# Optimization experiments

Hardware: AMD Instinct MI355X
Metric: run time of the kernel (lower is better)

## Reference

```python
import jax, jax.numpy as jnp
import numpy as np

B, T, C = 8, 2048, 1024


def setup_inputs() -> dict:
    key = jax.random.key(0)
    ks = jax.random.split(key, 7)
    s = 0.02  # typical init scale for weights
    return {
        "x": jax.random.normal(ks[0], (B, T, C), jnp.float32),
        "wq": jax.random.normal(ks[1], (C, C), jnp.float32) * s,
        "bq": jax.random.normal(ks[2], (C,), jnp.float32) * s,
        "wk": jax.random.normal(ks[3], (C, C), jnp.float32) * s,
        "bk": jax.random.normal(ks[4], (C,), jnp.float32) * s,
        "wv": jax.random.normal(ks[5], (C, C), jnp.float32) * s,
        "bv": jax.random.normal(ks[6], (C,), jnp.float32) * s,
    }


def reference(x, wq, bq, wk, bk, wv, bv):
    # x: [B, T, C]; torch Linear stores weight as [out, in] -> x @ W.T + b
    Bx, Tx, Cx = x.shape
    Q = x @ wq.T + bq  # [B, T, C]
    K = x @ wk.T + bk
    V = x @ wv.T + bv
    # NOTE: source computes K @ Q^T (keys index rows, queries index columns)
    scores = jnp.einsum("btc,bsc->bts", K, Q) / jnp.sqrt(jnp.float32(Cx))  # [B, T, T]
    causal = jnp.tril(jnp.ones((Tx, Tx), dtype=bool))  # mask==0 above diagonal
    scores = jnp.where(causal, scores, -jnp.inf)
    # torch masked_fill with a (1,1,T,T) mask broadcasts scores to (1,B,T,T)
    scores = scores[None]  # [1, B, T, T]
    w = jax.nn.softmax(scores, axis=-1)
    out = jnp.einsum("abts,bsc->abtc", w, V)  # [1, B, T, C]
    return out
```

## Files before the change

### kernel.cpp

```cpp
#include <hip/hip_runtime.h>
#include <stdint.h>

typedef unsigned short u16;
typedef __attribute__((ext_vector_type(8))) __bf16 bf16x8;
typedef __attribute__((ext_vector_type(4))) float f32x4;

#define DEVI __device__ __forceinline__

DEVI u16 f32_to_bf16(float f) {
  uint32_t u = __builtin_bit_cast(uint32_t, f);
  u += 0x7FFFu + ((u >> 16) & 1u);
  return (u16)(u >> 16);
}

DEVI void gl2lds16(const void* g, void* l) {
  __builtin_amdgcn_global_load_lds(
      (const __attribute__((address_space(1))) void*)g,
      (__attribute__((address_space(3))) void*)l, 16, 0, 0);
}

#define SMEM_U16 17408

#define S_BATCH 2228224

DEVI void gemm_bt_mainloop(const u16* __restrict__ A, const u16* __restrict__ B,
                           int lda, int ldb, int kIters,
                           u16* As, u16* Bs, f32x4 (&acc)[4][4]) {
  const int tid = threadIdx.x;
  const int lane = tid & 63;
  const int wid = tid >> 6;
  const int wr = wid >> 1, wc = wid & 1;
  const int l15 = lane & 15, quad = lane >> 4;

  const int srow = tid >> 3;
  const int sgrp = ((tid & 7) - srow) & 7;
  const u16* Ag = A + (size_t)srow * lda + sgrp * 8;
  const u16* Bg = B + (size_t)srow * ldb + sgrp * 8;
  char* AsDst = (char*)As + tid * 16;
  char* BsDst = (char*)Bs + tid * 16;

  const int a_row0 = wr * 64 + l15;
  const int b_row0 = wc * 64 + l15;

  for (int kb = 0; kb < kIters; ++kb) {
#pragma unroll
    for (int r = 0; r < 4; ++r) {
      gl2lds16(Ag + (size_t)(r * 32) * lda, AsDst + r * 4096);
      gl2lds16(Bg + (size_t)(r * 32) * ldb, BsDst + r * 4096);
    }
    Ag += 64;
    Bg += 64;
    __syncthreads();
#pragma unroll
    for (int kk = 0; kk < 2; ++kk) {
      const int gA = ((kk * 4 + quad + a_row0) & 7) * 8;
      const int gB = ((kk * 4 + quad + b_row0) & 7) * 8;
      bf16x8 af[4], bfr[4];
#pragma unroll
      for (int i = 0; i < 4; ++i)
        af[i] = *(const bf16x8*)(As + (a_row0 + i * 16) * 64 + gA);
#pragma unroll
      for (int j = 0; j < 4; ++j)
        bfr[j] = *(const bf16x8*)(Bs + (b_row0 + j * 16) * 64 + gB);
#pragma unroll
      for (int i = 0; i < 4; ++i)
#pragma unroll
        for (int j = 0; j < 4; ++j)
          acc[i][j] = __builtin_amdgcn_mfma_f32_16x16x32_bf16(af[i], bfr[j],
                                                              acc[i][j], 0, 0, 0);
    }
    __syncthreads();
  }
}

__global__ void cast_f32_to_bf16_kernel(const float* __restrict__ src,
                                        u16* __restrict__ dst, int n4) {
  int i = blockIdx.x * blockDim.x + threadIdx.x;
  const int stride = gridDim.x * blockDim.x;
  for (; i < n4; i += stride) {
    const float4 v = ((const float4*)src)[i];
    ushort4 o;
    o.x = f32_to_bf16(v.x);
    o.y = f32_to_bf16(v.y);
    o.z = f32_to_bf16(v.z);
    o.w = f32_to_bf16(v.w);
    ((ushort4*)dst)[i] = o;
  }
}

__global__ void cast_w_kernel(const float* __restrict__ wq,
                              const float* __restrict__ wk,
                              const float* __restrict__ wv,
                              u16* __restrict__ wb, float* __restrict__ sums) {
  const int z = blockIdx.y;
  if (z == 3) {
    int i = blockIdx.x * blockDim.x + threadIdx.x;
    if (i < 4096) ((float4*)sums)[i] = (float4){0.f, 0.f, 0.f, 0.f};
    return;
  }
  const float* src = (z == 0) ? wq : (z == 1) ? wk : wv;
  u16* dst = wb + (size_t)z * 1048576;
  int i = blockIdx.x * blockDim.x + threadIdx.x;
  const int stride = gridDim.x * blockDim.x;
  for (; i < 262144; i += stride) {
    const float4 v = ((const float4*)src)[i];
    ushort4 o;
    o.x = f32_to_bf16(v.x);
    o.y = f32_to_bf16(v.y);
    o.z = f32_to_bf16(v.z);
    o.w = f32_to_bf16(v.w);
    ((ushort4*)dst)[i] = o;
  }
}

__global__ __launch_bounds__(512, 2) void qkv_kernel(
    const u16* __restrict__ xb, const u16* __restrict__ wb,
    const float* __restrict__ bq, const float* __restrict__ bk,
    const float* __restrict__ bv, u16* __restrict__ Qb, u16* __restrict__ Kb,
    u16* __restrict__ Vt) {
  __shared__ __align__(16) u16 lds[65536];

  const int id = blockIdx.x;
  const int wg = (id & 7) * 96 + (id >> 3);
  const int g = wg >> 3, u = wg & 7;
  const int z = g >> 5;
  const int tp = g & 31;
  const int tmt = tp * 2 + (u >> 2);
  const int tct = u & 3;

  int m0, n0;
  const u16* Aptr;
  const u16* Bptr;
  if (z < 2) {
    m0 = tct * 256;
    n0 = tmt * 256;
    Aptr = wb + (size_t)z * 1048576 + (size_t)m0 * 1024;
    Bptr = xb + (size_t)n0 * 1024;
  } else {
    m0 = tmt * 256;
    n0 = tct * 256;
    Aptr = xb + (size_t)m0 * 1024;
    Bptr = wb + (size_t)2 * 1048576 + (size_t)n0 * 1024;
  }

  const int tid = threadIdx.x;
  const int srow = tid >> 3;
  const int sgrp = ((tid & 7) - srow) & 7;
  const u16* Ag = Aptr + (size_t)srow * 1024 + sgrp * 8;
  const u16* Bg = Bptr + (size_t)srow * 1024 + sgrp * 8;
  char* ldsDst = (char*)lds + tid * 16;

#define ST_A0(kt) do { const u16* s_ = Ag + (kt) * 64;           char* d_ = ldsDst + (((kt) & 1) * 65536);         gl2lds16(s_, d_); gl2lds16(s_ + 65536, d_ + 8192); } while (0)
#define ST_A1(kt) do { const u16* s_ = Ag + 131072 + (kt) * 64;  char* d_ = ldsDst + (((kt) & 1) * 65536) + 16384; gl2lds16(s_, d_); gl2lds16(s_ + 65536, d_ + 8192); } while (0)
#define ST_B0(kt) do { const u16* s_ = Bg + (kt) * 64;           char* d_ = ldsDst + (((kt) & 1) * 65536) + 32768; gl2lds16(s_, d_); gl2lds16(s_ + 65536, d_ + 8192); } while (0)
#define ST_B1(kt) do { const u16* s_ = Bg + 131072 + (kt) * 64;  char* d_ = ldsDst + (((kt) & 1) * 65536) + 49152; gl2lds16(s_, d_); gl2lds16(s_ + 65536, d_ + 8192); } while (0)

  ST_A0(0); ST_B0(0); ST_B1(0); ST_A1(0);
  ST_A0(1); ST_B0(1); ST_B1(1);

  const int lane = tid & 63, wid = tid >> 6;
  const int wr = wid >> 2, wc = wid & 3;
  const int l15 = lane & 15, quad = lane >> 4;

  int aoff[4][2], boff[2][2];
#pragma unroll
  for (int i_ = 0; i_ < 4; ++i_) {
    const int arow = wr * 64 + i_ * 16 + l15;
#pragma unroll
    for (int k_ = 0; k_ < 2; ++k_)
      aoff[i_][k_] = arow * 64 + ((k_ * 4 + quad + arow) & 7) * 8;
  }
#pragma unroll
  for (int j_ = 0; j_ < 2; ++j_) {
    const int brow = wc * 32 + j_ * 16 + l15;
#pragma unroll
    for (int k_ = 0; k_ < 2; ++k_)
      boff[j_][k_] = brow * 64 + ((k_ * 4 + quad + brow) & 7) * 8;
  }

  f32x4 acc[2][2][4][2];
#pragma unroll
  for (int a_ = 0; a_ < 2; ++a_)
#pragma unroll
    for (int b_ = 0; b_ < 2; ++b_)
#pragma unroll
      for (int i_ = 0; i_ < 4; ++i_)
#pragma unroll
        for (int j_ = 0; j_ < 2; ++j_)
          acc[a_][b_][i_][j_] = (f32x4){0.f, 0.f, 0.f, 0.f};

  bf16x8 af[4][2], bfr[2][2][2];

#define LOADA(qm, buf) do { const u16* p_ = lds + (buf) * 32768 + (qm) * 8192; \
  _Pragma("unroll") for (int i_ = 0; i_ < 4; ++i_) \
  _Pragma("unroll") for (int k_ = 0; k_ < 2; ++k_) \
    af[i_][k_] = *(const bf16x8*)(p_ + aoff[i_][k_]); } while (0)
#define LOADB(qn, buf) do { const u16* p_ = lds + (buf) * 32768 + 16384 + (qn) * 8192; \
  _Pragma("unroll") for (int j_ = 0; j_ < 2; ++j_) \
  _Pragma("unroll") for (int k_ = 0; k_ < 2; ++k_) \
    bfr[qn][j_][k_] = *(const bf16x8*)(p_ + boff[j_][k_]); } while (0)
#define MMA(qm, qn) do { \
  _Pragma("unroll") for (int i_ = 0; i_ < 4; ++i_) \
  _Pragma("unroll") for (int j_ = 0; j_ < 2; ++j_) \
  _Pragma("unroll") for (int k_ = 0; k_ < 2; ++k_) \
    acc[qm][qn][i_][j_] = __builtin_amdgcn_mfma_f32_16x16x32_bf16( \
        af[i_][k_], bfr[qn][j_][k_], acc[qm][qn][i_][j_], 0, 0, 0); } while (0)

#define BAR __builtin_amdgcn_s_barrier()
#define WLG0 asm volatile("s_waitcnt lgkmcnt(0)")
#define PRIO1 __builtin_amdgcn_s_setprio(1)
#define PRIO0 __builtin_amdgcn_s_setprio(0)
#define WVM6 asm volatile("s_waitcnt vmcnt(6)" ::: "memory")
#define WVM0 asm volatile("s_waitcnt vmcnt(0)" ::: "memory")

  WVM6;
  BAR;

#pragma unroll 1
  for (int it = 0; it < 7; ++it) {
    const int j0 = 2 * it;
    LOADA(0, 0); LOADB(0, 0); ST_A1(j0 + 1);
    BAR; WLG0; PRIO1; MMA(0, 0); PRIO0; LOADB(1, 0); BAR;
    ST_A0(j0 + 2);
    BAR; WLG0; PRIO1; MMA(0, 1); PRIO0; LOADA(1, 0); BAR;
    ST_B0(j0 + 2);
    BAR; WLG0; PRIO1; MMA(1, 1); PRIO0; BAR;
    ST_B1(j0 + 2);
    BAR; PRIO1; MMA(1, 0); PRIO0;
    WVM6;
    BAR;
    LOADA(0, 1); LOADB(0, 1); ST_A1(j0 + 2);
    BAR; WLG0; PRIO1; MMA(0, 0); PRIO0; LOADB(1, 1); BAR;
    ST_A0(j0 + 3);
    BAR; WLG0; PRIO1; MMA(0, 1); PRIO0; LOADA(1, 1); BAR;
    ST_B0(j0 + 3);
    BAR; WLG0; PRIO1; MMA(1, 1); PRIO0; BAR;
    ST_B1(j0 + 3);
    BAR; PRIO1; MMA(1, 0); PRIO0;
    WVM6;
    BAR;
  }
  {
    LOADA(0, 0); LOADB(0, 0); ST_A1(15);
    BAR; WLG0; PRIO1; MMA(0, 0); PRIO0; LOADB(1, 0); BAR;
    BAR; WLG0; PRIO1; MMA(0, 1); PRIO0; LOADA(1, 0); BAR;
    BAR; WLG0; PRIO1; MMA(1, 1); PRIO0; BAR;
    BAR; PRIO1; MMA(1, 0); PRIO0;
    WVM0;
    BAR;
    LOADA(0, 1); LOADB(0, 1);
    BAR; WLG0; PRIO1; MMA(0, 0); PRIO0; LOADB(1, 1); BAR;
    BAR; WLG0; PRIO1; MMA(0, 1); PRIO0; LOADA(1, 1); BAR;
    BAR; WLG0; PRIO1; MMA(1, 1); PRIO0; BAR;
    PRIO1; MMA(1, 0); PRIO0;
  }

  if (z < 2) {
    const float* bias = (z == 0) ? bq : bk;
    u16* Out = (z == 0) ? Qb : Kb;
#pragma unroll
    for (int th = 0; th < 2; ++th) {
      if (th) __syncthreads();
#pragma unroll
      for (int qm = 0; qm < 2; ++qm)
#pragma unroll
        for (int i_ = 0; i_ < 4; ++i_) {
          const int c = qm * 128 + wr * 64 + i_ * 16 + quad * 4;
          const float4 b4 = *(const float4*)(bias + m0 + c);
#pragma unroll
          for (int j_ = 0; j_ < 2; ++j_) {
            const int row = wc * 32 + j_ * 16 + l15;
            ushort4 o;
            o.x = f32_to_bf16(acc[qm][th][i_][j_][0] + b4.x);
            o.y = f32_to_bf16(acc[qm][th][i_][j_][1] + b4.y);
            o.z = f32_to_bf16(acc[qm][th][i_][j_][2] + b4.z);
            o.w = f32_to_bf16(acc[qm][th][i_][j_][3] + b4.w);
            *(ushort4*)(lds + row * 264 + c) = o;
          }
        }
      __syncthreads();
#pragma unroll
      for (int p = 0; p < 8; ++p) {
        const int row = p * 16 + (tid >> 5);
        const int c0 = (tid & 31) * 8;
        const uint4 v = *(const uint4*)(lds + row * 264 + c0);
        *(uint4*)(Out + (size_t)(n0 + th * 128 + row) * 1024 + m0 + c0) = v;
      }
    }
  } else {
    const int b = m0 >> 11;
    const int t0b = m0 & 2047;
    u16* Out = Vt + (size_t)b * 2097152;
#pragma unroll
    for (int th = 0; th < 2; ++th) {
      if (th) __syncthreads();
#pragma unroll
      for (int j_ = 0; j_ < 2; ++j_) {
        const int row = wc * 32 + j_ * 16 + l15;
        const float bb = bv[n0 + th * 128 + row];
#pragma unroll
        for (int qm = 0; qm < 2; ++qm)
#pragma unroll
          for (int i_ = 0; i_ < 4; ++i_) {
            const int c = qm * 128 + wr * 64 + i_ * 16 + quad * 4;
            ushort4 o;
            o.x = f32_to_bf16(acc[qm][th][i_][j_][0] + bb);
            o.y = f32_to_bf16(acc[qm][th][i_][j_][1] + bb);
            o.z = f32_to_bf16(acc[qm][th][i_][j_][2] + bb);
            o.w = f32_to_bf16(acc[qm][th][i_][j_][3] + bb);
            *(ushort4*)(lds + row * 264 + c) = o;
          }
      }
      __syncthreads();
#pragma unroll
      for (int p = 0; p < 8; ++p) {
        const int row = p * 16 + (tid >> 5);
        const int c0 = (tid & 31) * 8;
        const uint4 v = *(const uint4*)(lds + row * 264 + c0);
        *(uint4*)(Out + (size_t)(n0 + th * 128 + row) * 2048 + t0b + c0) = v;
      }
    }
  }
#undef ST_A0
#undef ST_A1
#undef ST_B0
#undef ST_B1
#undef LOADA
#undef LOADB
#undef MMA
#undef BAR
#undef WLG0
#undef PRIO1
#undef PRIO0
#undef WVM6
#undef WVM0
}

__global__ __launch_bounds__(512, 2) void score_kernel(const u16* __restrict__ Kb,
                                                       const u16* __restrict__ Qb,
                                                       u16* __restrict__ Spk,
                                                       float* __restrict__ sums) {
  __shared__ __align__(16) u16 lds[49152];

  const int id = blockIdx.x;
  const int b = id & 7;
  const int l = id >> 3;
  int k = (int)((sqrtf(4.f * l + 1.f) - 1.f) * 0.5f);
  if (k * (k + 1) > l) --k;
  if ((k + 1) * (k + 2) <= l) ++k;
  const int off = l - k * (k + 1);
  const int hi = (off >= (k + 1));
  const int rt = 2 * k + hi;
  const int ct = off - (hi ? (k + 1) : 0);
  const bool maskT = (ct == k);

  const int tid = threadIdx.x;
  const int srow = tid >> 3;
  const int sgrp = ((tid & 7) - srow) & 7;
  const u16* A = Qb + ((size_t)b * 2048 + ct * 256) * 1024;
  const u16* B = Kb + ((size_t)b * 2048 + rt * 128) * 1024;
  const u16* Ag = A + (size_t)srow * 1024 + sgrp * 8;
  const u16* Bg = B + (size_t)srow * 1024 + sgrp * 8;
  char* ldsDst = (char*)lds + tid * 16;

#define ST_A0(kt) do { const u16* s_ = Ag + (kt) * 64;           char* d_ = ldsDst + (((kt) & 1) * 49152);         gl2lds16(s_, d_); gl2lds16(s_ + 65536, d_ + 8192); } while (0)
#define ST_A1(kt) do { const u16* s_ = Ag + 131072 + (kt) * 64;  char* d_ = ldsDst + (((kt) & 1) * 49152) + 16384; gl2lds16(s_, d_); gl2lds16(s_ + 65536, d_ + 8192); } while (0)
#define ST_B(kt)  do { const u16* s_ = Bg + (kt) * 64;           char* d_ = ldsDst + (((kt) & 1) * 49152) + 32768; gl2lds16(s_, d_); gl2lds16(s_ + 65536, d_ + 8192); } while (0)

  ST_A0(0); ST_B(0); ST_A1(0);
  ST_A0(1); ST_B(1);

  const int lane = tid & 63, wid = tid >> 6;
  const int wr = wid >> 2, wc = wid & 3;
  const int l15 = lane & 15, quad = lane >> 4;

  int aoff[4][2], boff[2][2];
#pragma unroll
  for (int i_ = 0; i_ < 4; ++i_) {
    const int arow = wr * 64 + i_ * 16 + l15;
#pragma unroll
    for (int k_ = 0; k_ < 2; ++k_)
      aoff[i_][k_] = arow * 64 + ((k_ * 4 + quad + arow) & 7) * 8;
  }
#pragma unroll
  for (int j_ = 0; j_ < 2; ++j_) {
    const int brow = wc * 32 + j_ * 16 + l15;
#pragma unroll
    for (int k_ = 0; k_ < 2; ++k_)
      boff[j_][k_] = brow * 64 + ((k_ * 4 + quad + brow) & 7) * 8;
  }

  f32x4 acc[2][4][2];
#pragma unroll
  for (int q_ = 0; q_ < 2; ++q_)
#pragma unroll
    for (int i_ = 0; i_ < 4; ++i_)
#pragma unroll
      for (int j_ = 0; j_ < 2; ++j_)
        acc[q_][i_][j_] = (f32x4){0.f, 0.f, 0.f, 0.f};

  bf16x8 af[4][2], bfr[2][2];

#define SLOADA(qm, buf) do { const u16* p_ = lds + (buf) * 24576 + (qm) * 8192; \
  _Pragma("unroll") for (int i_ = 0; i_ < 4; ++i_) \
  _Pragma("unroll") for (int k_ = 0; k_ < 2; ++k_) \
    af[i_][k_] = *(const bf16x8*)(p_ + aoff[i_][k_]); } while (0)
#define SLOADB(buf) do { const u16* p_ = lds + (buf) * 24576 + 16384; \
  _Pragma("unroll") for (int j_ = 0; j_ < 2; ++j_) \
  _Pragma("unroll") for (int k_ = 0; k_ < 2; ++k_) \
    bfr[j_][k_] = *(const bf16x8*)(p_ + boff[j_][k_]); } while (0)
#define SMMA(qm) do { \
  _Pragma("unroll") for (int i_ = 0; i_ < 4; ++i_) \
  _Pragma("unroll") for (int j_ = 0; j_ < 2; ++j_) \
  _Pragma("unroll") for (int k_ = 0; k_ < 2; ++k_) \
    acc[qm][i_][j_] = __builtin_amdgcn_mfma_f32_16x16x32_bf16( \
        af[i_][k_], bfr[j_][k_], acc[qm][i_][j_], 0, 0, 0); } while (0)

#define BAR __builtin_amdgcn_s_barrier()
#define WLG0 asm volatile("s_waitcnt lgkmcnt(0)")
#define PRIO1 __builtin_amdgcn_s_setprio(1)
#define PRIO0 __builtin_amdgcn_s_setprio(0)
#define WVM4 asm volatile("s_waitcnt vmcnt(4)" ::: "memory")
#define WVM0 asm volatile("s_waitcnt vmcnt(0)" ::: "memory")

  WVM4;
  BAR;

#pragma unroll 1
  for (int it = 0; it < 7; ++it) {
    const int j0 = 2 * it;
    SLOADA(0, 0); SLOADB(0); ST_A1(j0 + 1);
    BAR; WLG0; PRIO1; SMMA(0); PRIO0; SLOADA(1, 0); BAR;
    ST_A0(j0 + 2); ST_B(j0 + 2);
    BAR; WLG0; PRIO1; SMMA(1); PRIO0;
    WVM4;
    BAR;
    SLOADA(0, 1); SLOADB(1); ST_A1(j0 + 2);
    BAR; WLG0; PRIO1; SMMA(0); PRIO0; SLOADA(1, 1); BAR;
    ST_A0(j0 + 3); ST_B(j0 + 3);
    BAR; WLG0; PRIO1; SMMA(1); PRIO0;
    WVM4;
    BAR;
  }
  {
    SLOADA(0, 0); SLOADB(0); ST_A1(15);
    BAR; WLG0; PRIO1; SMMA(0); PRIO0; SLOADA(1, 0); BAR;
    BAR; WLG0; PRIO1; SMMA(1); PRIO0;
    WVM0;
    BAR;
    SLOADA(0, 1); SLOADB(1);
    BAR; WLG0; PRIO1; SMMA(0); PRIO0; SLOADA(1, 1); BAR;
    BAR; WLG0; PRIO1; SMMA(1); PRIO0; BAR;
  }

  const int moff = (rt & 1) * 128;
  float sj[2] = {0.f, 0.f};
#pragma unroll
  for (int qm = 0; qm < 2; ++qm)
#pragma unroll
    for (int i_ = 0; i_ < 4; ++i_) {
      const int s0 = qm * 128 + wr * 64 + i_ * 16 + quad * 4;
#pragma unroll
      for (int j_ = 0; j_ < 2; ++j_) {
        const int t = wc * 32 + j_ * 16 + l15;
        ushort4 o;
        float e[4];
#pragma unroll
        for (int r = 0; r < 4; ++r) {
          float v = __expf(acc[qm][i_][j_][r] * 0.03125f);
          if (maskT && (s0 + r) > (t + moff)) v = 0.f;
          e[r] = v;
          sj[j_] += v;
        }
        o.x = f32_to_bf16(e[0]);
        o.y = f32_to_bf16(e[1]);
        o.z = f32_to_bf16(e[2]);
        o.w = f32_to_bf16(e[3]);
        *(ushort4*)(lds + t * 264 + s0) = o;
      }
    }
#pragma unroll
  for (int j_ = 0; j_ < 2; ++j_) {
    float v = sj[j_];
    v += __shfl_xor(v, 16);
    v += __shfl_xor(v, 32);
    if (quad == 0)
      atomicAdd(&sums[(size_t)b * 2048 + rt * 128 + wc * 32 + j_ * 16 + l15], v);
  }
  __syncthreads();
  const int ld = (rt + 1) * 128;
  const int nc = ld - ct * 256;
  u16* Out = Spk + (size_t)b * S_BATCH + (size_t)(rt * (rt + 1) / 2) * 16384 +
             ct * 256;
  if (nc >= 256) {
#pragma unroll
    for (int p = 0; p < 8; ++p) {
      const int row = p * 16 + (tid >> 5);
      const int c0 = (tid & 31) * 8;
      const uint4 v = *(const uint4*)(lds + row * 264 + c0);
      *(uint4*)(Out + (size_t)row * ld + c0) = v;
    }
  } else {
#pragma unroll
    for (int p = 0; p < 4; ++p) {
      const int row = p * 32 + (tid >> 4);
      const int c0 = (tid & 15) * 8;
      const uint4 v = *(const uint4*)(lds + row * 264 + c0);
      *(uint4*)(Out + (size_t)row * ld + c0) = v;
    }
  }
#undef ST_A0
#undef ST_A1
#undef ST_B
#undef SLOADA
#undef SLOADB
#undef SMMA
#undef BAR
#undef WLG0
#undef PRIO1
#undef PRIO0
#undef WVM4
#undef WVM0
}

__global__ __launch_bounds__(256) void pv_kernel(const u16* __restrict__ Spk,
                                                 const u16* __restrict__ Vt,
                                                 const float* __restrict__ sums,
                                                 float* __restrict__ Out) {
  const int b = blockIdx.x & 7;
  const int local = 127 - (blockIdx.x >> 3);
  const int rt = local >> 3;
  const int ct = local & 7;

  __shared__ __align__(16) u16 smem[SMEM_U16];
  u16* As = smem;
  u16* Bs = smem + 8192;
  float* ftile = (float*)smem;

  f32x4 acc[4][4];
#pragma unroll
  for (int i = 0; i < 4; ++i)
#pragma unroll
    for (int j = 0; j < 4; ++j) acc[i][j] = (f32x4){0.f, 0.f, 0.f, 0.f};

  const u16* A = Vt + ((size_t)b * 1024 + ct * 128) * 2048;
  const u16* B = Spk + (size_t)b * S_BATCH +
                 (size_t)(rt * (rt + 1) / 2) * 16384;
  const int ldb = (rt + 1) * 128;
  gemm_bt_mainloop(A, B, 2048, ldb, (rt + 1) * 2, As, Bs, acc);

  const int tid = threadIdx.x;
  const int lane = tid & 63, wid = tid >> 6;
  const int wr = wid >> 1, wc = wid & 1;
  const int l15 = lane & 15, quad = lane >> 4;

  const float* sumsb = sums + (size_t)b * 2048 + rt * 128;
  float* Ob = Out + (size_t)b * 2048 * 1024 + (size_t)(rt * 128) * 1024 +
              ct * 128;
#pragma unroll
  for (int h = 0; h < 2; ++h) {
    if (wc == h) {
#pragma unroll
      for (int j = 0; j < 4; ++j) {
        const int tl = j * 16 + l15;
        const float iv = 1.0f / sumsb[h * 64 + tl];
#pragma unroll
        for (int i = 0; i < 4; ++i) {
          const int c0 = wr * 64 + i * 16 + quad * 4;
          float4 v;
          v.x = acc[i][j][0] * iv;
          v.y = acc[i][j][1] * iv;
          v.z = acc[i][j][2] * iv;
          v.w = acc[i][j][3] * iv;
          *(float4*)(ftile + tl * 132 + c0) = v;
        }
      }
    }
    __syncthreads();
#pragma unroll
    for (int rr = 0; rr < 8; ++rr) {
      const int row = rr * 8 + (tid >> 5);
      const int c0 = (tid & 31) * 4;
      const float4 v = *(const float4*)(ftile + row * 132 + c0);
      *(float4*)(Ob + (size_t)(h * 64 + row) * 1024 + c0) = v;
    }
    __syncthreads();
  }
}

extern "C" void kernel_launch(void* const* d_in, const int* in_sizes, int n_in,
                              void* d_out, int out_size, void* d_ws,
                              size_t ws_size, hipStream_t stream) {
  const float* x = (const float*)d_in[0];
  const float* wq = (const float*)d_in[1];
  const float* bq = (const float*)d_in[2];
  const float* wk = (const float*)d_in[3];
  const float* bk = (const float*)d_in[4];
  const float* wv = (const float*)d_in[5];
  const float* bv = (const float*)d_in[6];
  float* out = (float*)d_out;
  char* ws = (char*)d_ws;

  u16* Qb = (u16*)(ws);
  u16* Kb = (u16*)(ws + ((size_t)32 << 20));
  u16* Vt = (u16*)(ws + ((size_t)64 << 20));
  u16* Spk = (u16*)(ws + ((size_t)96 << 20));
  u16* xb = (u16*)(ws + ((size_t)96 << 20));
  float* sums = (float*)(ws + ((size_t)132 << 20));
  u16* wb = (u16*)(ws + ((size_t)134 << 20));

  cast_f32_to_bf16_kernel<<<16384, 256, 0, stream>>>(x, xb, 16777216 / 4);
  cast_w_kernel<<<dim3(512, 4), 256, 0, stream>>>(wq, wk, wv, wb, sums);

  qkv_kernel<<<768, 512, 0, stream>>>(xb, wb, bq, bk, bv, Qb, Kb, Vt);

  score_kernel<<<576, 512, 0, stream>>>(Kb, Qb, Spk, sums);

  pv_kernel<<<8 * 128, 256, 0, stream>>>(Spk, Vt, sums, out);
}
```

Baseline: 333.3 us.

## Rewrite PV kernel as pipelined 256x128 tile GEMM and reschedule LDS reads

The PV kernel is rewritten. The old version used 256-thread blocks with 128x128 tiles and a single-buffered mainloop. The new one uses 512-thread blocks with 256x128 tiles, double-buffered direct global-to-LDS loads, the vmcnt/barrier/priority pipelined schedule already used by the score kernel, and a paired heavy/light rt ordering across the grid. In the QKV and score kernels, LDS fragment reads for the next MMA now issue after the barrier instead of inside the priority-1 MMA section, with a partial lgkmcnt wait added. The intent is to overlap memory with MFMA and raise reuse in PV, at the cost of fewer, larger blocks and more register pressure.

```diff
diff --git a/kernel.cpp b/kernel.cpp
--- a/kernel.cpp
+++ b/kernel.cpp
@@ -19,59 +19,7 @@
       (__attribute__((address_space(3))) void*)l, 16, 0, 0);
 }
 
-#define SMEM_U16 17408
-
 #define S_BATCH 2228224
-
-DEVI void gemm_bt_mainloop(const u16* __restrict__ A, const u16* __restrict__ B,
-                           int lda, int ldb, int kIters,
-                           u16* As, u16* Bs, f32x4 (&acc)[4][4]) {
-  const int tid = threadIdx.x;
-  const int lane = tid & 63;
-  const int wid = tid >> 6;
-  const int wr = wid >> 1, wc = wid & 1;
-  const int l15 = lane & 15, quad = lane >> 4;
-
-  const int srow = tid >> 3;
-  const int sgrp = ((tid & 7) - srow) & 7;
-  const u16* Ag = A + (size_t)srow * lda + sgrp * 8;
-  const u16* Bg = B + (size_t)srow * ldb + sgrp * 8;
-  char* AsDst = (char*)As + tid * 16;
-  char* BsDst = (char*)Bs + tid * 16;
-
-  const int a_row0 = wr * 64 + l15;
-  const int b_row0 = wc * 64 + l15;
-
-  for (int kb = 0; kb < kIters; ++kb) {
-#pragma unroll
-    for (int r = 0; r < 4; ++r) {
-      gl2lds16(Ag + (size_t)(r * 32) * lda, AsDst + r * 4096);
-      gl2lds16(Bg + (size_t)(r * 32) * ldb, BsDst + r * 4096);
-    }
-    Ag += 64;
-    Bg += 64;
-    __syncthreads();
-#pragma unroll
-    for (int kk = 0; kk < 2; ++kk) {
-      const int gA = ((kk * 4 + quad + a_row0) & 7) * 8;
-      const int gB = ((kk * 4 + quad + b_row0) & 7) * 8;
-      bf16x8 af[4], bfr[4];
-#pragma unroll
-      for (int i = 0; i < 4; ++i)
-        af[i] = *(const bf16x8*)(As + (a_row0 + i * 16) * 64 + gA);
-#pragma unroll
-      for (int j = 0; j < 4; ++j)
-        bfr[j] = *(const bf16x8*)(Bs + (b_row0 + j * 16) * 64 + gB);
-#pragma unroll
-      for (int i = 0; i < 4; ++i)
-#pragma unroll
-        for (int j = 0; j < 4; ++j)
-          acc[i][j] = __builtin_amdgcn_mfma_f32_16x16x32_bf16(af[i], bfr[j],
-                                                              acc[i][j], 0, 0, 0);
-    }
-    __syncthreads();
-  }
-}
 
 __global__ void cast_f32_to_bf16_kernel(const float* __restrict__ src,
                                         u16* __restrict__ dst, int n4) {
@@ -208,6 +156,7 @@
 
 #define BAR __builtin_amdgcn_s_barrier()
 #define WLG0 asm volatile("s_waitcnt lgkmcnt(0)")
+#define WLG8 asm volatile("s_waitcnt lgkmcnt(8)")
 #define PRIO1 __builtin_amdgcn_s_setprio(1)
 #define PRIO0 __builtin_amdgcn_s_setprio(0)
 #define WVM6 asm volatile("s_waitcnt vmcnt(6)" ::: "memory")
@@ -219,21 +168,21 @@
 #pragma unroll 1
   for (int it = 0; it < 7; ++it) {
     const int j0 = 2 * it;
-    LOADA(0, 0); LOADB(0, 0); ST_A1(j0 + 1);
-    BAR; WLG0; PRIO1; MMA(0, 0); PRIO0; LOADB(1, 0); BAR;
-    ST_A0(j0 + 2);
-    BAR; WLG0; PRIO1; MMA(0, 1); PRIO0; LOADA(1, 0); BAR;
-    ST_B0(j0 + 2);
+    LOADA(0, 0); LOADB(0, 0); ST_A1(j0 + 1); WLG8;
+    BAR; WLG0; PRIO1; MMA(0, 0); PRIO0; BAR;
+    LOADB(1, 0); ST_A0(j0 + 2);
+    BAR; WLG0; PRIO1; MMA(0, 1); PRIO0; BAR;
+    LOADA(1, 0); ST_B0(j0 + 2);
     BAR; WLG0; PRIO1; MMA(1, 1); PRIO0; BAR;
     ST_B1(j0 + 2);
     BAR; PRIO1; MMA(1, 0); PRIO0;
     WVM6;
     BAR;
-    LOADA(0, 1); LOADB(0, 1); ST_A1(j0 + 2);
-    BAR; WLG0; PRIO1; MMA(0, 0); PRIO0; LOADB(1, 1); BAR;
-    ST_A0(j0 + 3);
-    BAR; WLG0; PRIO1; MMA(0, 1); PRIO0; LOADA(1, 1); BAR;
-    ST_B0(j0 + 3);
+    LOADA(0, 1); LOADB(0, 1); ST_A1(j0 + 2); WLG8;
+    BAR; WLG0; PRIO1; MMA(0, 0); PRIO0; BAR;
+    LOADB(1, 1); ST_A0(j0 + 3);
+    BAR; WLG0; PRIO1; MMA(0, 1); PRIO0; BAR;
+    LOADA(1, 1); ST_B0(j0 + 3);
     BAR; WLG0; PRIO1; MMA(1, 1); PRIO0; BAR;
     ST_B1(j0 + 3);
     BAR; PRIO1; MMA(1, 0); PRIO0;
@@ -241,18 +190,23 @@
     BAR;
   }
   {
-    LOADA(0, 0); LOADB(0, 0); ST_A1(15);
-    BAR; WLG0; PRIO1; MMA(0, 0); PRIO0; LOADB(1, 0); BAR;
-    BAR; WLG0; PRIO1; MMA(0, 1); PRIO0; LOADA(1, 0); BAR;
+    LOADA(0, 0); LOADB(0, 0); ST_A1(15); WLG8;
+    BAR; WLG0; PRIO1; MMA(0, 0); PRIO0; BAR;
+    LOADB(1, 0);
+    BAR; WLG0; PRIO1; MMA(0, 1); PRIO0; BAR;
+    LOADA(1, 0);
     BAR; WLG0; PRIO1; MMA(1, 1); PRIO0; BAR;
     BAR; PRIO1; MMA(1, 0); PRIO0;
     WVM0;
     BAR;
-    LOADA(0, 1); LOADB(0, 1);
-    BAR; WLG0; PRIO1; MMA(0, 0); PRIO0; LOADB(1, 1); BAR;
-    BAR; WLG0; PRIO1; MMA(0, 1); PRIO0; LOADA(1, 1); BAR;
+    LOADA(0, 1); LOADB(0, 1); WLG8;
+    BAR; WLG0; PRIO1; MMA(0, 0); PRIO0; BAR;
+    LOADB(1, 1);
+    BAR; WLG0; PRIO1; MMA(0, 1); PRIO0; BAR;
+    LOADA(1, 1);
     BAR; WLG0; PRIO1; MMA(1, 1); PRIO0; BAR;
     PRIO1; MMA(1, 0); PRIO0;
+    BAR;
   }
 
   if (z < 2) {
@@ -330,6 +284,7 @@
 #undef MMA
 #undef BAR
 #undef WLG0
+#undef WLG8
 #undef PRIO1
 #undef PRIO0
 #undef WVM6
@@ -430,26 +385,28 @@
   for (int it = 0; it < 7; ++it) {
     const int j0 = 2 * it;
     SLOADA(0, 0); SLOADB(0); ST_A1(j0 + 1);
-    BAR; WLG0; PRIO1; SMMA(0); PRIO0; SLOADA(1, 0); BAR;
-    ST_A0(j0 + 2); ST_B(j0 + 2);
+    BAR; WLG0; PRIO1; SMMA(0); PRIO0; BAR;
+    SLOADA(1, 0); ST_A0(j0 + 2); ST_B(j0 + 2);
     BAR; WLG0; PRIO1; SMMA(1); PRIO0;
     WVM4;
     BAR;
     SLOADA(0, 1); SLOADB(1); ST_A1(j0 + 2);
-    BAR; WLG0; PRIO1; SMMA(0); PRIO0; SLOADA(1, 1); BAR;
-    ST_A0(j0 + 3); ST_B(j0 + 3);
+    BAR; WLG0; PRIO1; SMMA(0); PRIO0; BAR;
+    SLOADA(1, 1); ST_A0(j0 + 3); ST_B(j0 + 3);
     BAR; WLG0; PRIO1; SMMA(1); PRIO0;
     WVM4;
     BAR;
   }
   {
     SLOADA(0, 0); SLOADB(0); ST_A1(15);
-    BAR; WLG0; PRIO1; SMMA(0); PRIO0; SLOADA(1, 0); BAR;
+    BAR; WLG0; PRIO1; SMMA(0); PRIO0; BAR;
+    SLOADA(1, 0);
     BAR; WLG0; PRIO1; SMMA(1); PRIO0;
     WVM0;
     BAR;
     SLOADA(0, 1); SLOADB(1);
-    BAR; WLG0; PRIO1; SMMA(0); PRIO0; SLOADA(1, 1); BAR;
+    BAR; WLG0; PRIO1; SMMA(0); PRIO0; BAR;
+    SLOADA(1, 1);
     BAR; WLG0; PRIO1; SMMA(1); PRIO0; BAR;
   }
 
@@ -523,69 +480,170 @@
 #undef WVM0
 }
 
-__global__ __launch_bounds__(256) void pv_kernel(const u16* __restrict__ Spk,
-                                                 const u16* __restrict__ Vt,
-                                                 const float* __restrict__ sums,
-                                                 float* __restrict__ Out) {
-  const int b = blockIdx.x & 7;
-  const int local = 127 - (blockIdx.x >> 3);
-  const int rt = local >> 3;
-  const int ct = local & 7;
-
-  __shared__ __align__(16) u16 smem[SMEM_U16];
-  u16* As = smem;
-  u16* Bs = smem + 8192;
-  float* ftile = (float*)smem;
-
-  f32x4 acc[4][4];
-#pragma unroll
-  for (int i = 0; i < 4; ++i)
-#pragma unroll
-    for (int j = 0; j < 4; ++j) acc[i][j] = (f32x4){0.f, 0.f, 0.f, 0.f};
-
-  const u16* A = Vt + ((size_t)b * 1024 + ct * 128) * 2048;
+__global__ __launch_bounds__(512, 2) void pv_kernel(const u16* __restrict__ Spk,
+                                                    const u16* __restrict__ Vt,
+                                                    const float* __restrict__ sums,
+                                                    float* __restrict__ Out) {
+  __shared__ __align__(16) u16 lds[49152];
+
+  const int id = blockIdx.x;
+  const int hf = id >> 8;
+  const int rr_ = id & 255;
+  const int rt = hf ? (rr_ >> 5) : 15 - (rr_ >> 5);
+  const int ct = (rr_ >> 3) & 3;
+  const int b = rr_ & 7;
+
+  const int ldb = (rt + 1) * 128;
+  const int nk2 = rt + 1;
+
+  const int tid = threadIdx.x;
+  const int srow = tid >> 3;
+  const int sgrp = ((tid & 7) - srow) & 7;
+  const u16* A = Vt + ((size_t)b * 1024 + ct * 256) * 2048;
   const u16* B = Spk + (size_t)b * S_BATCH +
                  (size_t)(rt * (rt + 1) / 2) * 16384;
-  const int ldb = (rt + 1) * 128;
-  gemm_bt_mainloop(A, B, 2048, ldb, (rt + 1) * 2, As, Bs, acc);
-
-  const int tid = threadIdx.x;
+  const u16* Ag = A + (size_t)srow * 2048 + sgrp * 8;
+  const u16* Bg = B + (size_t)srow * ldb + sgrp * 8;
+  char* ldsDst = (char*)lds + tid * 16;
+
+#define ST_A0(kt) do { const u16* s_ = Ag + (kt) * 64;            char* d_ = ldsDst + (((kt) & 1) * 49152);         gl2lds16(s_, d_); gl2lds16(s_ + 131072, d_ + 8192); } while (0)
+#define ST_A1(kt) do { const u16* s_ = Ag + 262144 + (kt) * 64;   char* d_ = ldsDst + (((kt) & 1) * 49152) + 16384; gl2lds16(s_, d_); gl2lds16(s_ + 131072, d_ + 8192); } while (0)
+#define ST_B(kt)  do { const u16* s_ = Bg + (kt) * 64;            char* d_ = ldsDst + (((kt) & 1) * 49152) + 32768; gl2lds16(s_, d_); gl2lds16(s_ + (size_t)64 * ldb, d_ + 8192); } while (0)
+
+  ST_A0(0); ST_B(0); ST_A1(0);
+  ST_A0(1); ST_B(1);
+
   const int lane = tid & 63, wid = tid >> 6;
-  const int wr = wid >> 1, wc = wid & 1;
+  const int wr = wid >> 2, wc = wid & 3;
   const int l15 = lane & 15, quad = lane >> 4;
 
+  int aoff[4][2], boff[2][2];
+#pragma unroll
+  for (int i_ = 0; i_ < 4; ++i_) {
+    const int arow = wr * 64 + i_ * 16 + l15;
+#pragma unroll
+    for (int k_ = 0; k_ < 2; ++k_)
+      aoff[i_][k_] = arow * 64 + ((k_ * 4 + quad + arow) & 7) * 8;
+  }
+#pragma unroll
+  for (int j_ = 0; j_ < 2; ++j_) {
+    const int brow = wc * 32 + j_ * 16 + l15;
+#pragma unroll
+    for (int k_ = 0; k_ < 2; ++k_)
+      boff[j_][k_] = brow * 64 + ((k_ * 4 + quad + brow) & 7) * 8;
+  }
+
+  f32x4 acc[2][4][2];
+#pragma unroll
+  for (int q_ = 0; q_ < 2; ++q_)
+#pragma unroll
+    for (int i_ = 0; i_ < 4; ++i_)
+#pragma unroll
+      for (int j_ = 0; j_ < 2; ++j_)
+        acc[q_][i_][j_] = (f32x4){0.f, 0.f, 0.f, 0.f};
+
+  bf16x8 af[4][2], bfr[2][2];
+
+#define SLOADA(qm, buf) do { const u16* p_ = lds + (buf) * 24576 + (qm) * 8192; \
+  _Pragma("unroll") for (int i_ = 0; i_ < 4; ++i_) \
+  _Pragma("unroll") for (int k_ = 0; k_ < 2; ++k_) \
+    af[i_][k_] = *(const bf16x8*)(p_ + aoff[i_][k_]); } while (0)
+#define SLOADB(buf) do { const u16* p_ = lds + (buf) * 24576 + 16384; \
+  _Pragma("unroll") for (int j_ = 0; j_ < 2; ++j_) \
+  _Pragma("unroll") for (int k_ = 0; k_ < 2; ++k_) \
+    bfr[j_][k_] = *(const bf16x8*)(p_ + boff[j_][k_]); } while (0)
+#define SMMA(qm) do { \
+  _Pragma("unroll") for (int i_ = 0; i_ < 4; ++i_) \
+  _Pragma("unroll") for (int j_ = 0; j_ < 2; ++j_) \
+  _Pragma("unroll") for (int k_ = 0; k_ < 2; ++k_) \
+    acc[qm][i_][j_] = __builtin_amdgcn_mfma_f32_16x16x32_bf16( \
+        af[i_][k_], bfr[j_][k_], acc[qm][i_][j_], 0, 0, 0); } while (0)
+
+#define BAR __builtin_amdgcn_s_barrier()
+#define WLG0 asm volatile("s_waitcnt lgkmcnt(0)")
+#define PRIO1 __builtin_amdgcn_s_setprio(1)
+#define PRIO0 __builtin_amdgcn_s_setprio(0)
+#define WVM4 asm volatile("s_waitcnt vmcnt(4)" ::: "memory")
+#define WVM0 asm volatile("s_waitcnt vmcnt(0)" ::: "memory")
+
+  WVM4;
+  BAR;
+
+#pragma unroll 1
+  for (int it = 0; it < nk2 - 1; ++it) {
+    const int j0 = 2 * it;
+    SLOADA(0, 0); SLOADB(0); ST_A1(j0 + 1);
+    BAR; WLG0; PRIO1; SMMA(0); PRIO0; BAR;
+    SLOADA(1, 0); ST_A0(j0 + 2); ST_B(j0 + 2);
+    BAR; WLG0; PRIO1; SMMA(1); PRIO0;
+    WVM4;
+    BAR;
+    SLOADA(0, 1); SLOADB(1); ST_A1(j0 + 2);
+    BAR; WLG0; PRIO1; SMMA(0); PRIO0; BAR;
+    SLOADA(1, 1); ST_A0(j0 + 3); ST_B(j0 + 3);
+    BAR; WLG0; PRIO1; SMMA(1); PRIO0;
+    WVM4;
+    BAR;
+  }
+  {
+    SLOADA(0, 0); SLOADB(0); ST_A1(2 * nk2 - 1);
+    BAR; WLG0; PRIO1; SMMA(0); PRIO0; BAR;
+    SLOADA(1, 0);
+    BAR; WLG0; PRIO1; SMMA(1); PRIO0;
+    WVM0;
+    BAR;
+    SLOADA(0, 1); SLOADB(1);
+    BAR; WLG0; PRIO1; SMMA(0); PRIO0; BAR;
+    SLOADA(1, 1);
+    BAR; WLG0; PRIO1; SMMA(1); PRIO0; BAR;
+  }
+
+  float* ftile = (float*)lds;
   const float* sumsb = sums + (size_t)b * 2048 + rt * 128;
   float* Ob = Out + (size_t)b * 2048 * 1024 + (size_t)(rt * 128) * 1024 +
-              ct * 128;
-#pragma unroll
-  for (int h = 0; h < 2; ++h) {
-    if (wc == h) {
-#pragma unroll
-      for (int j = 0; j < 4; ++j) {
-        const int tl = j * 16 + l15;
-        const float iv = 1.0f / sumsb[h * 64 + tl];
-#pragma unroll
-        for (int i = 0; i < 4; ++i) {
-          const int c0 = wr * 64 + i * 16 + quad * 4;
-          float4 v;
-          v.x = acc[i][j][0] * iv;
-          v.y = acc[i][j][1] * iv;
-          v.z = acc[i][j][2] * iv;
-          v.w = acc[i][j][3] * iv;
-          *(float4*)(ftile + tl * 132 + c0) = v;
-        }
+              ct * 256;
+  float iv[2];
+#pragma unroll
+  for (int j_ = 0; j_ < 2; ++j_)
+    iv[j_] = 1.0f / sumsb[wc * 32 + j_ * 16 + l15];
+#pragma unroll
+  for (int qm = 0; qm < 2; ++qm) {
+    if (qm) __syncthreads();
+#pragma unroll
+    for (int i_ = 0; i_ < 4; ++i_) {
+      const int c0 = wr * 64 + i_ * 16 + quad * 4;
+#pragma unroll
+      for (int j_ = 0; j_ < 2; ++j_) {
+        const int t = wc * 32 + j_ * 16 + l15;
+        float4 v;
+        v.x = acc[qm][i_][j_][0] * iv[j_];
+        v.y = acc[qm][i_][j_][1] * iv[j_];
+        v.z = acc[qm][i_][j_][2] * iv[j_];
+        v.w = acc[qm][i_][j_][3] * iv[j_];
+        *(float4*)(ftile + t * 132 + c0) = v;
       }
     }
     __syncthreads();
 #pragma unroll
-    for (int rr = 0; rr < 8; ++rr) {
-      const int row = rr * 8 + (tid >> 5);
-      const int c0 = (tid & 31) * 4;
-      const float4 v = *(const float4*)(ftile + row * 132 + c0);
-      *(float4*)(Ob + (size_t)(h * 64 + row) * 1024 + c0) = v;
+    for (int p = 0; p < 8; ++p) {
+      const int row = p * 16 + (tid >> 5);
+      const int c0f = (tid & 31) * 4;
+      const float4 v = *(const float4*)(ftile + row * 132 + c0f);
+      *(float4*)(Ob + (size_t)row * 1024 + qm * 128 + c0f) = v;
     }
-    __syncthreads();
-  }
+  }
+#undef ST_A0
+#undef ST_A1
+#undef ST_B
+#undef SLOADA
+#undef SLOADB
+#undef SMMA
+#undef BAR
+#undef WLG0
+#undef PRIO1
+#undef PRIO0
+#undef WVM4
+#undef WVM0
 }
 
 extern "C" void kernel_launch(void* const* d_in, const int* in_sizes, int n_in,
@@ -616,5 +674,5 @@
 
   score_kernel<<<576, 512, 0, stream>>>(Kb, Qb, Spk, sums);
 
-  pv_kernel<<<8 * 128, 256, 0, stream>>>(Spk, Vt, sums, out);
-}
+  pv_kernel<<<512, 512, 0, stream>>>(Spk, Vt, sums, out);
+}
```

After: 331.8 us. About the same (-0.4%).
